# Kernel tuning notes

Measured on AMD Instinct MI355X. Metric: run time of the kernel, lower is better.

The kernel has to match this reference:

```python
import jax, jax.numpy as jnp
import numpy as np

N_GAUSS = 2_000_000
N_VERTS = 5023
N_FACES = 9976


def _safe_normalize(x, eps=1e-20):
    return x / jnp.sqrt(jnp.clip(jnp.sum(x * x, axis=-1, keepdims=True), eps, None))


def _rotmat_to_unitquat_xyzw(R):
    # scipy/roma-style branchless rotation-matrix -> unit quaternion (xyzw)
    r00, r01, r02 = R[..., 0, 0], R[..., 0, 1], R[..., 0, 2]
    r10, r11, r12 = R[..., 1, 0], R[..., 1, 1], R[..., 1, 2]
    r20, r21, r22 = R[..., 2, 0], R[..., 2, 1], R[..., 2, 2]
    t = r00 + r11 + r22
    qx = jnp.stack([1 + r00 - r11 - r22, r10 + r01, r20 + r02, r21 - r12], -1)
    qy = jnp.stack([r10 + r01, 1 - r00 + r11 - r22, r21 + r12, r02 - r20], -1)
    qz = jnp.stack([r20 + r02, r21 + r12, 1 - r00 - r11 + r22, r10 - r01], -1)
    qw = jnp.stack([r21 - r12, r02 - r20, r10 - r01, 1 + t], -1)
    decision = jnp.stack([r00, r11, r22, t], -1)
    choice = jnp.argmax(decision, axis=-1)[..., None]
    q = jnp.where(choice == 0, qx, jnp.where(choice == 1, qy, jnp.where(choice == 2, qz, qw)))
    return q / jnp.linalg.norm(q, axis=-1, keepdims=True)


def _quat_product_xyzw(p, q):
    pv, pw = p[..., :3], p[..., 3:4]
    qv, qw = q[..., :3], q[..., 3:4]
    v = pw * qv + qw * pv + jnp.cross(pv, qv)
    w = pw * qw - jnp.sum(pv * qv, axis=-1, keepdims=True)
    return jnp.concatenate([v, w], axis=-1)


def _xyzw_to_wxyz(q):
    return jnp.concatenate([q[..., 3:4], q[..., :3]], axis=-1)


def _wxyz_to_xyzw(q):
    return jnp.concatenate([q[..., 1:4], q[..., 0:1]], axis=-1)


def setup_inputs() -> dict:
    key = jax.random.key(0)
    ks = jax.random.split(key, 9)
    return {
        'verts': jax.random.normal(ks[0], (N_VERTS, 3), jnp.float32),
        'xyz': jax.random.normal(ks[1], (N_GAUSS, 3), jnp.float32),
        'opacity_raw': jax.random.normal(ks[2], (N_GAUSS, 1), jnp.float32),
        'scaling_raw': jax.random.normal(ks[3], (N_GAUSS, 3), jnp.float32),
        'rotation_raw': jax.random.normal(ks[4], (N_GAUSS, 4), jnp.float32),
        'features_dc': jax.random.normal(ks[5], (N_GAUSS, 1, 3), jnp.float32),
        'features_rest': jax.random.normal(ks[6], (N_GAUSS, 15, 3), jnp.float32),
        'faces': jax.random.randint(ks[7], (N_FACES, 3), 0, N_VERTS, jnp.int32),
        'binding': jax.random.randint(ks[8], (N_GAUSS,), 0, N_FACES, jnp.int32),
    }


def reference(verts, xyz, opacity_raw, scaling_raw, rotation_raw, features_dc, features_rest, faces, binding):
    # ---- per-face quantities (small: F ~= 10k) ----
    tri = verts[faces]                         # [F,3,3]
    face_center = tri.mean(axis=1)             # [F,3]
    v0, v1, v2 = tri[:, 0], tri[:, 1], tri[:, 2]
    a0 = _safe_normalize(v1 - v0)
    c = jnp.cross(a0, v2 - v0)
    a1 = _safe_normalize(c)
    a2 = -_safe_normalize(jnp.cross(a1, a0))
    R = jnp.stack([a0, a1, a2], axis=-1)       # [F,3,3], columns = tangent frame
    s0 = jnp.linalg.norm(v1 - v0, axis=-1, keepdims=True)
    s1 = jnp.abs(jnp.sum(c * a1, axis=-1, keepdims=True))
    face_scaling = (s0 + s1) / 2               # [F,1]
    face_quat_wxyz = _xyzw_to_wxyz(_rotmat_to_unitquat_xyzw(R))  # [F,4]

    # ---- per-Gaussian hot path: gather + 3x3 matvec + quat compose ----
    Rb = R[binding]                            # [N,3,3]
    fs = face_scaling[binding]                 # [N,1]
    g_xyz = jnp.einsum('nij,nj->ni', Rb, xyz) * fs + face_center[binding]  # [N,3]
    opacity = jax.nn.sigmoid(opacity_raw)      # [N,1]
    scales = jnp.exp(scaling_raw) * fs         # [N,3]
    rot = rotation_raw / (jnp.sqrt(jnp.sum(rotation_raw ** 2, axis=1, keepdims=True)) + 1e-12)
    fq = face_quat_wxyz[binding]
    fq = fq / (jnp.sqrt(jnp.sum(fq ** 2, axis=1, keepdims=True)) + 1e-12)
    rotations = _xyzw_to_wxyz(_quat_product_xyzw(_wxyz_to_xyzw(fq), _wxyz_to_xyzw(rot)))
    # shs = cat(features_dc, features_rest)[:, 0] == features_dc[:, 0]
    shs0 = features_dc[:, 0, :]
    color = jnp.clip(jnp.concatenate([0.5 + 0.282 * shs0, opacity], axis=-1) * 255.0, 0.0, 255.0)
    rotations = rotations / jnp.linalg.norm(rotations, axis=-1, keepdims=True)
    return jnp.concatenate([g_xyz, scales, color, rotations], axis=-1)  # [N,14]


if __name__ == '__main__':
    out = reference(**setup_inputs())
    print(out.shape, out.dtype)
```

## Files before the change

### kernel.cpp

```cpp
#include <hip/hip_runtime.h>
#include <math.h>


typedef float f32x4 __attribute__((ext_vector_type(4)));

__device__ __forceinline__ float fast_exp(float x) {
    return __builtin_amdgcn_exp2f(x * 1.4426950408889634f);
}
__device__ __forceinline__ float fast_rcp(float x) {
    return __builtin_amdgcn_rcpf(x);
}
__device__ __forceinline__ float fast_rsq(float x) {
    return __builtin_amdgcn_rsqf(x);
}

struct F3 { float x, y, z; };
__device__ __forceinline__ F3 mkf3(float x, float y, float z) { F3 r; r.x = x; r.y = y; r.z = z; return r; }
__device__ __forceinline__ F3 f3sub(F3 a, F3 b) { return mkf3(a.x - b.x, a.y - b.y, a.z - b.z); }
__device__ __forceinline__ F3 f3add(F3 a, F3 b) { return mkf3(a.x + b.x, a.y + b.y, a.z + b.z); }
__device__ __forceinline__ F3 f3scl(F3 a, float s) { return mkf3(a.x * s, a.y * s, a.z * s); }
__device__ __forceinline__ float f3dot(F3 a, F3 b) { return a.x * b.x + a.y * b.y + a.z * b.z; }
__device__ __forceinline__ F3 f3cross(F3 a, F3 b) {
    return mkf3(a.y * b.z - a.z * b.y, a.z * b.x - a.x * b.z, a.x * b.y - a.y * b.x);
}

__device__ void face_geom(const float* __restrict__ verts, const int* __restrict__ faces, int f,
                          F3& a0, F3& a1, F3& a2, F3& ctr, float& fs, float4& quat_wxyz)
{
    int i0 = faces[3 * f + 0], i1 = faces[3 * f + 1], i2 = faces[3 * f + 2];
    F3 v0 = mkf3(verts[3 * i0], verts[3 * i0 + 1], verts[3 * i0 + 2]);
    F3 v1 = mkf3(verts[3 * i1], verts[3 * i1 + 1], verts[3 * i1 + 2]);
    F3 v2 = mkf3(verts[3 * i2], verts[3 * i2 + 1], verts[3 * i2 + 2]);

    ctr = f3scl(f3add(f3add(v0, v1), v2), (1.0f / 3.0f));

    F3 e1 = f3sub(v1, v0);
    float d1 = f3dot(e1, e1);
    float s0 = sqrtf(d1);
    a0 = f3scl(e1, 1.0f / sqrtf(fmaxf(d1, 1e-20f)));

    F3 e2 = f3sub(v2, v0);
    F3 c = f3cross(a0, e2);
    float dc = f3dot(c, c);
    a1 = f3scl(c, 1.0f / sqrtf(fmaxf(dc, 1e-20f)));

    F3 c2 = f3cross(a1, a0);
    float dc2 = f3dot(c2, c2);
    F3 n2 = f3scl(c2, 1.0f / sqrtf(fmaxf(dc2, 1e-20f)));
    a2 = mkf3(-n2.x, -n2.y, -n2.z);

    float s1 = fabsf(f3dot(c, a1));
    fs = 0.5f * (s0 + s1);

    float r00 = a0.x, r10 = a0.y, r20 = a0.z;
    float r01 = a1.x, r11 = a1.y, r21 = a1.z;
    float r02 = a2.x, r12 = a2.y, r22 = a2.z;
    float t = r00 + r11 + r22;

    float cand[4][4] = {
        { 1.0f + r00 - r11 - r22, r10 + r01,              r20 + r02,              r21 - r12 },
        { r10 + r01,              1.0f - r00 + r11 - r22, r21 + r12,              r02 - r20 },
        { r20 + r02,              r21 + r12,              1.0f - r00 - r11 + r22, r10 - r01 },
        { r21 - r12,              r02 - r20,              r10 - r01,              1.0f + t  }
    };
    float dec[4] = { r00, r11, r22, t };
    int ch = 0;
    float best = dec[0];
#pragma unroll
    for (int j = 1; j < 4; ++j) {
        if (dec[j] > best) { best = dec[j]; ch = j; }
    }
    float qx = cand[ch][0], qy = cand[ch][1], qz = cand[ch][2], qw = cand[ch][3];
    float inv = 1.0f / sqrtf(qx * qx + qy * qy + qz * qz + qw * qw);
    quat_wxyz = make_float4(qw * inv, qx * inv, qy * inv, qz * inv);
}

__global__ __launch_bounds__(64)
void face_kernel2(const float* __restrict__ verts, const int* __restrict__ faces,
                  f32x4* __restrict__ fd, int nf)
{
    int f = blockIdx.x * 64 + threadIdx.x;
    if (f >= nf) return;
    F3 a0, a1, a2, ctr; float fs; float4 quat;
    face_geom(verts, faces, f, a0, a1, a2, ctr, fs, quat);
    f32x4 q; q.x = quat.x; q.y = quat.y; q.z = quat.z; q.w = quat.w;
    f32x4 c; c.x = ctr.x;  c.y = ctr.y;  c.z = ctr.z;  c.w = fs;
    fd[2 * f + 0] = q;
    fd[2 * f + 1] = c;
}

__global__ __launch_bounds__(256)
void gauss_q(const float* __restrict__ xyz, const float* __restrict__ opa,
             const float* __restrict__ scl, const f32x4* __restrict__ rot_raw,
             const float* __restrict__ fdc, const int* __restrict__ binding,
             const f32x4* __restrict__ face, float* __restrict__ out, int n)
{
    __shared__ float s_out[256 * 15];

    int tid = threadIdx.x;
    int g0  = blockIdx.x * 256;
    int cnt = n - g0; if (cnt > 256) cnt = 256;

    if (tid < cnt) {
        int i = g0 + tid;
        int b = binding[i];
        f32x4 q4 = face[2 * b + 0];
        f32x4 cf = face[2 * b + 1];
        float qw = q4.x, qx = q4.y, qy = q4.z, qz = q4.w;
        float fs = cf.w;

        float xx = qx * qx, yy = qy * qy, zz = qz * qz;
        float xy = qx * qy, xz = qx * qz, yz = qy * qz;
        float wx = qw * qx, wy = qw * qy, wz = qw * qz;
        float r00 = 1.0f - 2.0f * (yy + zz), r01 = 2.0f * (xy - wz), r02 = 2.0f * (xz + wy);
        float r10 = 2.0f * (xy + wz), r11 = 1.0f - 2.0f * (xx + zz), r12 = 2.0f * (yz - wx);
        float r20 = 2.0f * (xz - wy), r21 = 2.0f * (yz + wx), r22 = 1.0f - 2.0f * (xx + yy);

        float x = xyz[3 * i + 0], y = xyz[3 * i + 1], z = xyz[3 * i + 2];
        float gx = (r00 * x + r01 * y + r02 * z) * fs + cf.x;
        float gy = (r10 * x + r11 * y + r12 * z) * fs + cf.y;
        float gz = (r20 * x + r21 * y + r22 * z) * fs + cf.z;

        float s0 = fast_exp(scl[3 * i + 0]) * fs;
        float s1 = fast_exp(scl[3 * i + 1]) * fs;
        float s2 = fast_exp(scl[3 * i + 2]) * fs;

        float o = fast_rcp(1.0f + fast_exp(-opa[i]));

        f32x4 r = rot_raw[i];
        float rinv = fast_rcp(sqrtf(r.x * r.x + r.y * r.y + r.z * r.z + r.w * r.w) + 1e-12f);
        float rw = r.x * rinv, rx = r.y * rinv, ry = r.z * rinv, rz = r.w * rinv;

        float vx = qw * rx + rw * qx + (qy * rz - qz * ry);
        float vy = qw * ry + rw * qy + (qz * rx - qx * rz);
        float vz = qw * rz + rw * qz + (qx * ry - qy * rx);
        float vw = qw * rw - (qx * rx + qy * ry + qz * rz);
        float qinv = fast_rsq(vx * vx + vy * vy + vz * vz + vw * vw);

        float d0 = fdc[3 * i + 0], d1 = fdc[3 * i + 1], d2 = fdc[3 * i + 2];
        float c0 = fminf(fmaxf((0.5f + 0.282f * d0) * 255.0f, 0.0f), 255.0f);
        float c1 = fminf(fmaxf((0.5f + 0.282f * d1) * 255.0f, 0.0f), 255.0f);
        float c2 = fminf(fmaxf((0.5f + 0.282f * d2) * 255.0f, 0.0f), 255.0f);
        float c3 = fminf(fmaxf(o * 255.0f, 0.0f), 255.0f);

        float* po = &s_out[tid * 15];
        po[0]  = gx;        po[1]  = gy;        po[2]  = gz;
        po[3]  = s0;        po[4]  = s1;        po[5]  = s2;
        po[6]  = c0;        po[7]  = c1;        po[8]  = c2;        po[9] = c3;
        po[10] = vw * qinv; po[11] = vx * qinv; po[12] = vy * qinv; po[13] = vz * qinv;
    }
    __syncthreads();

    int nflo = cnt * 14;
    int nfo4 = nflo >> 2;
    f32x4* o4 = (f32x4*)(out + (size_t)g0 * 14);
    for (int j = tid; j < nfo4; j += 256) {
        int fb = 4 * j;
        int q  = fb / 14;
        int rr = fb - q * 14;
        int base = q * 15 + rr;
        f32x4 v;
        v.x = s_out[base];
        v.y = s_out[base + 1 + (rr >= 13 ? 1 : 0)];
        v.z = s_out[base + 2 + (rr >= 12 ? 1 : 0)];
        v.w = s_out[base + 3 + (rr >= 11 ? 1 : 0)];
        __builtin_nontemporal_store(v, o4 + j);
    }
    for (int f = (nfo4 << 2) + tid; f < nflo; f += 256) {
        __builtin_nontemporal_store(s_out[(f / 14) * 15 + f % 14],
                                    out + (size_t)g0 * 14 + f);
    }
}

__global__ __launch_bounds__(256)
void gauss_fused(const float* __restrict__ verts, const int* __restrict__ faces,
                 const float* __restrict__ xyz, const float* __restrict__ opa,
                 const float* __restrict__ scl, const f32x4* __restrict__ rot_raw,
                 const float* __restrict__ fdc, const int* __restrict__ binding,
                 float* __restrict__ out, int n)
{
    int i = blockIdx.x * 256 + threadIdx.x;
    if (i >= n) return;
    int b = binding[i];
    F3 a0, a1, a2, ctr; float fs; float4 quat;
    face_geom(verts, faces, b, a0, a1, a2, ctr, fs, quat);

    float x = xyz[3 * i], y = xyz[3 * i + 1], z = xyz[3 * i + 2];
    float gx = (a0.x * x + a1.x * y + a2.x * z) * fs + ctr.x;
    float gy = (a0.y * x + a1.y * y + a2.y * z) * fs + ctr.y;
    float gz = (a0.z * x + a1.z * y + a2.z * z) * fs + ctr.z;
    float s0 = expf(scl[3 * i + 0]) * fs;
    float s1 = expf(scl[3 * i + 1]) * fs;
    float s2 = expf(scl[3 * i + 2]) * fs;
    float o = 1.0f / (1.0f + expf(-opa[i]));
    f32x4 r = rot_raw[i];
    float rinv = 1.0f / (sqrtf(r.x * r.x + r.y * r.y + r.z * r.z + r.w * r.w) + 1e-12f);
    float rw = r.x * rinv, rx = r.y * rinv, ry = r.z * rinv, rz = r.w * rinv;
    float pw = quat.x, px = quat.y, py = quat.z, pz = quat.w;
    float vx = pw * rx + rw * px + (py * rz - pz * ry);
    float vy = pw * ry + rw * py + (pz * rx - px * rz);
    float vz = pw * rz + rw * pz + (px * ry - py * rx);
    float vw = pw * rw - (px * rx + py * ry + pz * rz);
    float qinv = 1.0f / sqrtf(vx * vx + vy * vy + vz * vz + vw * vw);
    float* po = out + (size_t)i * 14;
    po[0] = gx; po[1] = gy; po[2] = gz;
    po[3] = s0; po[4] = s1; po[5] = s2;
    po[6] = fminf(fmaxf((0.5f + 0.282f * fdc[3 * i + 0]) * 255.0f, 0.0f), 255.0f);
    po[7] = fminf(fmaxf((0.5f + 0.282f * fdc[3 * i + 1]) * 255.0f, 0.0f), 255.0f);
    po[8] = fminf(fmaxf((0.5f + 0.282f * fdc[3 * i + 2]) * 255.0f, 0.0f), 255.0f);
    po[9] = fminf(fmaxf(o * 255.0f, 0.0f), 255.0f);
    po[10] = vw * qinv; po[11] = vx * qinv; po[12] = vy * qinv; po[13] = vz * qinv;
}

extern "C" void kernel_launch(void* const* d_in, const int* in_sizes, int n_in,
                              void* d_out, int out_size, void* d_ws, size_t ws_size,
                              hipStream_t stream)
{
    const float* verts   = (const float*)d_in[0];
    const float* xyz     = (const float*)d_in[1];
    const float* opa     = (const float*)d_in[2];
    const float* scl     = (const float*)d_in[3];
    const float* rot     = (const float*)d_in[4];
    const float* fdc     = (const float*)d_in[5];
    const int*   faces   = (const int*)d_in[7];
    const int*   binding = (const int*)d_in[8];

    int n      = in_sizes[8];
    int nfaces = in_sizes[7] / 3;
    float* out = (float*)d_out;

    size_t need = (size_t)nfaces * 2 * sizeof(f32x4);

    if (ws_size >= need) {
        f32x4* face = (f32x4*)d_ws;
        hipLaunchKernelGGL(face_kernel2, dim3((nfaces + 63) / 64), dim3(64), 0, stream,
                           verts, faces, face, nfaces);
        hipLaunchKernelGGL(gauss_q, dim3((n + 255) / 256), dim3(256), 0, stream,
                           xyz, opa, scl, (const f32x4*)rot, fdc, binding, face, out, n);
    } else {
        hipLaunchKernelGGL(gauss_fused, dim3((n + 255) / 256), dim3(256), 0, stream,
                           verts, faces, xyz, opa, scl, (const f32x4*)rot, fdc, binding, out, n);
    }
}
```

Before: 43.52 us.

## Fuse face geometry computation into per-Gaussian kernel, drop face precompute pass

Removes the separate per-face kernel and its workspace buffer, and recomputes face frame, center, scale and quaternion inline for each Gaussian from verts and faces. This eliminates one kernel launch and the intermediate face table write/read. In exchange, each Gaussian now does dependent index-then-vertex gathers and extra sqrt/normalization math, increasing latency and register pressure in a bandwidth-bound kernel.

Result: slower. 50.75 us (+16.6%).

```diff
diff --git a/kernel.cpp b/kernel.cpp
--- a/kernel.cpp
+++ b/kernel.cpp
@@ -24,8 +24,10 @@
     return mkf3(a.y * b.z - a.z * b.y, a.z * b.x - a.x * b.z, a.x * b.y - a.y * b.x);
 }
 
-__device__ void face_geom(const float* __restrict__ verts, const int* __restrict__ faces, int f,
-                          F3& a0, F3& a1, F3& a2, F3& ctr, float& fs, float4& quat_wxyz)
+__device__ __forceinline__ void face_geom(const float* __restrict__ verts,
+                                          const int* __restrict__ faces, int f,
+                                          F3& a0, F3& a1, F3& a2, F3& ctr,
+                                          float& fs, float4& quat_wxyz)
 {
     int i0 = faces[3 * f + 0], i1 = faces[3 * f + 1], i2 = faces[3 * f + 2];
     F3 v0 = mkf3(verts[3 * i0], verts[3 * i0 + 1], verts[3 * i0 + 2]);
@@ -75,25 +77,12 @@
     quat_wxyz = make_float4(qw * inv, qx * inv, qy * inv, qz * inv);
 }
 
-__global__ __launch_bounds__(64)
-void face_kernel2(const float* __restrict__ verts, const int* __restrict__ faces,
-                  f32x4* __restrict__ fd, int nf)
-{
-    int f = blockIdx.x * 64 + threadIdx.x;
-    if (f >= nf) return;
-    F3 a0, a1, a2, ctr; float fs; float4 quat;
-    face_geom(verts, faces, f, a0, a1, a2, ctr, fs, quat);
-    f32x4 q; q.x = quat.x; q.y = quat.y; q.z = quat.z; q.w = quat.w;
-    f32x4 c; c.x = ctr.x;  c.y = ctr.y;  c.z = ctr.z;  c.w = fs;
-    fd[2 * f + 0] = q;
-    fd[2 * f + 1] = c;
-}
-
 __global__ __launch_bounds__(256)
-void gauss_q(const float* __restrict__ xyz, const float* __restrict__ opa,
-             const float* __restrict__ scl, const f32x4* __restrict__ rot_raw,
-             const float* __restrict__ fdc, const int* __restrict__ binding,
-             const f32x4* __restrict__ face, float* __restrict__ out, int n)
+void gauss_all(const float* __restrict__ verts, const int* __restrict__ faces,
+               const float* __restrict__ xyz, const float* __restrict__ opa,
+               const float* __restrict__ scl, const f32x4* __restrict__ rot_raw,
+               const float* __restrict__ fdc, const int* __restrict__ binding,
+               float* __restrict__ out, int n)
 {
     __shared__ float s_out[256 * 15];
 
@@ -103,41 +92,37 @@
 
     if (tid < cnt) {
         int i = g0 + tid;
-        int b = binding[i];
-        f32x4 q4 = face[2 * b + 0];
-        f32x4 cf = face[2 * b + 1];
-        float qw = q4.x, qx = q4.y, qy = q4.z, qz = q4.w;
-        float fs = cf.w;
 
-        float xx = qx * qx, yy = qy * qy, zz = qz * qz;
-        float xy = qx * qy, xz = qx * qz, yz = qy * qz;
-        float wx = qw * qx, wy = qw * qy, wz = qw * qz;
-        float r00 = 1.0f - 2.0f * (yy + zz), r01 = 2.0f * (xy - wz), r02 = 2.0f * (xz + wy);
-        float r10 = 2.0f * (xy + wz), r11 = 1.0f - 2.0f * (xx + zz), r12 = 2.0f * (yz - wx);
-        float r20 = 2.0f * (xz - wy), r21 = 2.0f * (yz + wx), r22 = 1.0f - 2.0f * (xx + yy);
+        float x  = xyz[3 * i + 0], y = xyz[3 * i + 1], z = xyz[3 * i + 2];
+        float sc0 = scl[3 * i + 0], sc1 = scl[3 * i + 1], sc2 = scl[3 * i + 2];
+        float d0 = fdc[3 * i + 0], d1 = fdc[3 * i + 1], d2 = fdc[3 * i + 2];
+        float op = opa[i];
+        f32x4 r  = rot_raw[i];
+        int b    = binding[i];
 
-        float x = xyz[3 * i + 0], y = xyz[3 * i + 1], z = xyz[3 * i + 2];
-        float gx = (r00 * x + r01 * y + r02 * z) * fs + cf.x;
-        float gy = (r10 * x + r11 * y + r12 * z) * fs + cf.y;
-        float gz = (r20 * x + r21 * y + r22 * z) * fs + cf.z;
+        F3 a0, a1, a2, ctr; float fs; float4 fq;
+        face_geom(verts, faces, b, a0, a1, a2, ctr, fs, fq);
 
-        float s0 = fast_exp(scl[3 * i + 0]) * fs;
-        float s1 = fast_exp(scl[3 * i + 1]) * fs;
-        float s2 = fast_exp(scl[3 * i + 2]) * fs;
+        float gx = (a0.x * x + a1.x * y + a2.x * z) * fs + ctr.x;
+        float gy = (a0.y * x + a1.y * y + a2.y * z) * fs + ctr.y;
+        float gz = (a0.z * x + a1.z * y + a2.z * z) * fs + ctr.z;
 
-        float o = fast_rcp(1.0f + fast_exp(-opa[i]));
+        float s0 = fast_exp(sc0) * fs;
+        float s1 = fast_exp(sc1) * fs;
+        float s2 = fast_exp(sc2) * fs;
 
-        f32x4 r = rot_raw[i];
+        float o = fast_rcp(1.0f + fast_exp(-op));
+
         float rinv = fast_rcp(sqrtf(r.x * r.x + r.y * r.y + r.z * r.z + r.w * r.w) + 1e-12f);
         float rw = r.x * rinv, rx = r.y * rinv, ry = r.z * rinv, rz = r.w * rinv;
 
-        float vx = qw * rx + rw * qx + (qy * rz - qz * ry);
-        float vy = qw * ry + rw * qy + (qz * rx - qx * rz);
-        float vz = qw * rz + rw * qz + (qx * ry - qy * rx);
-        float vw = qw * rw - (qx * rx + qy * ry + qz * rz);
+        float pw = fq.x, px = fq.y, py = fq.z, pz = fq.w;
+        float vx = pw * rx + rw * px + (py * rz - pz * ry);
+        float vy = pw * ry + rw * py + (pz * rx - px * rz);
+        float vz = pw * rz + rw * pz + (px * ry - py * rx);
+        float vw = pw * rw - (px * rx + py * ry + pz * rz);
         float qinv = fast_rsq(vx * vx + vy * vy + vz * vz + vw * vw);
 
-        float d0 = fdc[3 * i + 0], d1 = fdc[3 * i + 1], d2 = fdc[3 * i + 2];
         float c0 = fminf(fmaxf((0.5f + 0.282f * d0) * 255.0f, 0.0f), 255.0f);
         float c1 = fminf(fmaxf((0.5f + 0.282f * d1) * 255.0f, 0.0f), 255.0f);
         float c2 = fminf(fmaxf((0.5f + 0.282f * d2) * 255.0f, 0.0f), 255.0f);
@@ -172,46 +157,6 @@
     }
 }
 
-__global__ __launch_bounds__(256)
-void gauss_fused(const float* __restrict__ verts, const int* __restrict__ faces,
-                 const float* __restrict__ xyz, const float* __restrict__ opa,
-                 const float* __restrict__ scl, const f32x4* __restrict__ rot_raw,
-                 const float* __restrict__ fdc, const int* __restrict__ binding,
-                 float* __restrict__ out, int n)
-{
-    int i = blockIdx.x * 256 + threadIdx.x;
-    if (i >= n) return;
-    int b = binding[i];
-    F3 a0, a1, a2, ctr; float fs; float4 quat;
-    face_geom(verts, faces, b, a0, a1, a2, ctr, fs, quat);
-
-    float x = xyz[3 * i], y = xyz[3 * i + 1], z = xyz[3 * i + 2];
-    float gx = (a0.x * x + a1.x * y + a2.x * z) * fs + ctr.x;
-    float gy = (a0.y * x + a1.y * y + a2.y * z) * fs + ctr.y;
-    float gz = (a0.z * x + a1.z * y + a2.z * z) * fs + ctr.z;
-    float s0 = expf(scl[3 * i + 0]) * fs;
-    float s1 = expf(scl[3 * i + 1]) * fs;
-    float s2 = expf(scl[3 * i + 2]) * fs;
-    float o = 1.0f / (1.0f + expf(-opa[i]));
-    f32x4 r = rot_raw[i];
-    float rinv = 1.0f / (sqrtf(r.x * r.x + r.y * r.y + r.z * r.z + r.w * r.w) + 1e-12f);
-    float rw = r.x * rinv, rx = r.y * rinv, ry = r.z * rinv, rz = r.w * rinv;
-    float pw = quat.x, px = quat.y, py = quat.z, pz = quat.w;
-    float vx = pw * rx + rw * px + (py * rz - pz * ry);
-    float vy = pw * ry + rw * py + (pz * rx - px * rz);
-    float vz = pw * rz + rw * pz + (px * ry - py * rx);
-    float vw = pw * rw - (px * rx + py * ry + pz * rz);
-    float qinv = 1.0f / sqrtf(vx * vx + vy * vy + vz * vz + vw * vw);
-    float* po = out + (size_t)i * 14;
-    po[0] = gx; po[1] = gy; po[2] = gz;
-    po[3] = s0; po[4] = s1; po[5] = s2;
-    po[6] = fminf(fmaxf((0.5f + 0.282f * fdc[3 * i + 0]) * 255.0f, 0.0f), 255.0f);
-    po[7] = fminf(fmaxf((0.5f + 0.282f * fdc[3 * i + 1]) * 255.0f, 0.0f), 255.0f);
-    po[8] = fminf(fmaxf((0.5f + 0.282f * fdc[3 * i + 2]) * 255.0f, 0.0f), 255.0f);
-    po[9] = fminf(fmaxf(o * 255.0f, 0.0f), 255.0f);
-    po[10] = vw * qinv; po[11] = vx * qinv; po[12] = vy * qinv; po[13] = vz * qinv;
-}
-
 extern "C" void kernel_launch(void* const* d_in, const int* in_sizes, int n_in,
                               void* d_out, int out_size, void* d_ws, size_t ws_size,
                               hipStream_t stream)
@@ -225,20 +170,9 @@
     const int*   faces   = (const int*)d_in[7];
     const int*   binding = (const int*)d_in[8];
 
-    int n      = in_sizes[8];
-    int nfaces = in_sizes[7] / 3;
+    int n = in_sizes[8];
     float* out = (float*)d_out;
 
-    size_t need = (size_t)nfaces * 2 * sizeof(f32x4);
-
-    if (ws_size >= need) {
-        f32x4* face = (f32x4*)d_ws;
-        hipLaunchKernelGGL(face_kernel2, dim3((nfaces + 63) / 64), dim3(64), 0, stream,
-                           verts, faces, face, nfaces);
-        hipLaunchKernelGGL(gauss_q, dim3((n + 255) / 256), dim3(256), 0, stream,
-                           xyz, opa, scl, (const f32x4*)rot, fdc, binding, face, out, n);
-    } else {
-        hipLaunchKernelGGL(gauss_fused, dim3((n + 255) / 256), dim3(256), 0, stream,
-                           verts, faces, xyz, opa, scl, (const f32x4*)rot, fdc, binding, out, n);
-    }
+    hipLaunchKernelGGL(gauss_all, dim3((n + 255) / 256), dim3(256), 0, stream,
+                       verts, faces, xyz, opa, scl, (const f32x4*)rot, fdc, binding, out, n);
 }
```
